# Kernel tuning notes

Hardware: AMD Instinct MI355X
Metric: run time of the kernel (lower is better)

## Reference

```python
import jax, jax.numpy as jnp
import numpy as np

SIGNAL = (32, 32)
KERNEL = (8, 8)
N_FEATURES = [64, 128, 128]
BATCH = 64
ALPHA = 0.5          # source references an undefined global `alpha`; fixed here
LEAKY_SLOPE = 0.01   # torch F.leaky_relu default


def _join_tensor(S, K, loc):
    i = np.arange(S)[:, None, None]
    j = np.arange(S)[None, :, None]
    k = np.arange(K)[None, None, :]
    M = (j >= i) & (i == np.maximum(j, k + loc))
    return jnp.asarray(M.astype(np.float32))


def _meet_tensor(S, K, loc):
    i = np.arange(S)[:, None, None]
    j = np.arange(S)[None, :, None]
    k = np.arange(K)[None, None, :]
    M = (j >= i) & (i == np.minimum(j, k + loc))
    return jnp.asarray(M.astype(np.float32))


def setup_inputs() -> dict:
    key = jax.random.key(0)
    sx, sy = SIGNAL
    kx, ky = KERNEL
    # meet layers use kernel_loc = signal - kernel; join layers use (0, 0)
    cmx = _meet_tensor(sx, kx, sx - kx)
    cmy = _meet_tensor(sy, ky, sy - ky)
    cjx = _join_tensor(sx, kx, 0)
    cjy = _join_tensor(sy, ky, 0)

    keys = jax.random.split(key, 16)
    x = jax.random.normal(keys[0], (BATCH, N_FEATURES[0], sx, sy), dtype=jnp.float32)

    def kaiming(k, shape):
        fan_in = shape[0] * shape[1] * shape[2]  # kx*ky*in_features
        return jax.random.normal(k, shape, dtype=jnp.float32) * np.float32(np.sqrt(2.0 / fan_in))

    inp = {"x": x, "cmx": cmx, "cmy": cmy, "cjx": cjx, "cjy": cjy}
    for li in range(len(N_FEATURES) - 1):
        fi, fo = N_FEATURES[li], N_FEATURES[li + 1]
        inp[f"mw{li}"] = kaiming(keys[1 + 2 * li], (kx, ky, fi, fo))
        inp[f"mb{li}"] = jnp.zeros((fo, 1, 1), dtype=jnp.float32)
        inp[f"jw{li}"] = kaiming(keys[2 + 2 * li], (kx, ky, fi, fo))
        inp[f"jb{li}"] = jnp.zeros((fo, 1, 1), dtype=jnp.float32)
    return inp


def _lattice_conv(cx, cy, X, W, b):
    # Y[m,g,x,y] = sum_{i,j,a,b} cx[i,x,a] cy[j,y,b] X[m,f,i,j] W[a,b,f,g] + bias
    return jnp.einsum('ixa,jyb,mfij,abfg->mgxy', cx, cy, X, W, optimize='optimal') + b


def reference(x, cmx, cmy, cjx, cjy, mw0, mb0, jw0, jb0, mw1, mb1, jw1, jb1):
    params = [(mw0, mb0, jw0, jb0), (mw1, mb1, jw1, jb1)]
    for mw, mb, jw, jb in params:
        m = _lattice_conv(cmx, cmy, x, mw, mb)
        j = _lattice_conv(cjx, cjy, x, jw, jb)
        x = jax.nn.leaky_relu((1.0 - ALPHA) * m + ALPHA * j, negative_slope=LEAKY_SLOPE)
    return x
```

## Files before the change

kernel.cpp:

```cpp
#include <hip/hip_runtime.h>
#include <stdint.h>


typedef __attribute__((ext_vector_type(8))) short short8;
typedef __attribute__((ext_vector_type(4))) float floatx4;

__device__ __forceinline__ float bf2f(unsigned short u) {
  union { uint32_t u; float f; } c; c.u = ((uint32_t)u) << 16; return c.f;
}
__device__ __forceinline__ unsigned short f2bf(float f) {
  union { float f; uint32_t u; } c; c.f = f;
  uint32_t u = c.u;
  uint32_t r = (u + 0x7FFFu + ((u >> 16) & 1u)) >> 16;
  return (unsigned short)r;
}

__device__ __forceinline__ int detect_fp32_block(
    const unsigned short* __restrict__ xa, int* scnt) {
  if (threadIdx.x == 0) *scnt = 0;
  __syncthreads();
  unsigned short v = xa[threadIdx.x & 255];
  int e = (v >> 7) & 0xFF;
  int ok = (v == 0) || (e >= 110 && e <= 140);
  atomicAdd(scnt, ok);
  __syncthreads();
  return (*scnt >= 240) ? 0 : 1;
}

#define SLOT_W1 0
#define SLOT_SB 225
#define SLOT_AS 289
#define SLOT_M  353
#define N_SLOTS 417
#define N_SLOTS_PAD 448

__global__ __launch_bounds__(256) void mega_setup(
    const unsigned short* __restrict__ xa,
    const void* __restrict__ mw0, const void* __restrict__ jw0,
    const void* __restrict__ mw1, const void* __restrict__ jw1,
    const void* __restrict__ mb0, const void* __restrict__ jb0,
    const void* __restrict__ mb1, const void* __restrict__ jb1,
    unsigned short* __restrict__ L, float* __restrict__ bias0,
    float* __restrict__ bias1, unsigned short* __restrict__ PBg0,
    unsigned short* __restrict__ PBg1, unsigned short* __restrict__ Xt0) {
  __shared__ unsigned short shbuf[128 * 33];
  __shared__ int scnt;
  int blk = blockIdx.x;

  if (blk < 224) {
    int tid = blk * 256 + threadIdx.x;
    int slot = tid >> 7, k = tid & 127;
    int isj = k >= 64, ab = k & 63, a = ab >> 3, b = ab & 7;
    float v = 0.f;
    if (slot < 225) {
      int cx = slot / 15, cy = slot % 15;
      int pmx = cx < 7 ? cx : 7, pxx = cx > 7 ? cx - 7 : 0;
      int pmy = cy < 7 ? cy : 7, pyy = cy > 7 ? cy - 7 : 0;
      if (!isj) v = (a >= pxx && b >= pyy) ? 0.5f : 0.f;
      else      v = (a <= pmx && b <= pmy) ? 0.5f : 0.f;
    } else if (slot < 289) {
      int s = slot - SLOT_SB, px = s >> 3, b0 = s & 7;
      if (!isj) v = (a >= px && b == b0) ? 0.5f : 0.f;
    } else if (slot < 353) {
      int s = slot - SLOT_AS, a0 = s >> 3, py = s & 7;
      if (!isj) v = (a == a0 && b >= py) ? 0.5f : 0.f;
    } else if (slot < 417) {
      int s = slot - SLOT_M, a0 = s >> 3, b0 = s & 7;
      if (!isj) v = (a == a0 && b == b0) ? 0.5f : 0.f;
    }
    L[tid] = f2bf(v);
    return;
  }

  if (blk == 224) {
    int fp32 = detect_fp32_block(xa, &scnt);
    int g = threadIdx.x & 127;
    const void* mb = (threadIdx.x < 128) ? mb0 : mb1;
    const void* jb = (threadIdx.x < 128) ? jb0 : jb1;
    float* bo = (threadIdx.x < 128) ? bias0 : bias1;
    float m = fp32 ? ((const float*)mb)[g] : bf2f(((const unsigned short*)mb)[g]);
    float j = fp32 ? ((const float*)jb)[g] : bf2f(((const unsigned short*)jb)[g]);
    bo[g] = 0.5f * (m + j);
    return;
  }

  int tx = threadIdx.x & 31, ty = threadIdx.x >> 5;

  if (blk < 1249) {
    int fp32 = detect_fp32_block(xa, &scnt);
    int pblk = blk - 225;
    int layer = pblk >> 9;
    int rem = pblk & 511;
    int f = rem >> 2, gt = rem & 3;
    int F = layer ? 128 : 64;
    if (f >= F) return;
    int g0 = gt * 32;
    const int G = 128, FG = F * G;
    const void* mw = layer ? mw1 : mw0;
    const void* jw = layer ? jw1 : jw0;
    unsigned short* PB = layer ? PBg1 : PBg0;
    for (int k = ty; k < 128; k += 8) {
      const void* src = (k < 64) ? mw : jw;
      int ab = k & 63;
      size_t idx = (size_t)ab * FG + (size_t)f * G + g0 + tx;
      shbuf[k * 33 + tx] = fp32 ? f2bf(((const float*)src)[idx])
                                : ((const unsigned short*)src)[idx];
    }
    __syncthreads();
    int kk = threadIdx.x & 127, gs = threadIdx.x >> 7;
    for (int gg = gs; gg < 32; gg += 2)
      PB[((size_t)(g0 + gg) * F + f) * 128 + kk] = shbuf[kk * 33 + gg];
    return;
  }

  {
    int fp32 = detect_fp32_block(xa, &scnt);
    int tblk = blk - 1249;
    int c0 = (tblk & 31) * 32, r0 = (tblk >> 5) * 32;
    const int R = 4096, C = 1024;
    if (fp32) {
#pragma unroll
      for (int i = 0; i < 32; i += 8)
        shbuf[(ty + i) * 33 + tx] =
            f2bf(((const float*)xa)[(size_t)(r0 + ty + i) * C + (c0 + tx)]);
    } else {
#pragma unroll
      for (int i = 0; i < 32; i += 8)
        shbuf[(ty + i) * 33 + tx] = xa[(size_t)(r0 + ty + i) * C + (c0 + tx)];
    }
    __syncthreads();
#pragma unroll
    for (int i = 0; i < 32; i += 8)
      Xt0[(size_t)(c0 + ty + i) * R + (r0 + tx)] = shbuf[tx * 33 + ty + i];
  }
}

template <int F, int NT>
__device__ __forceinline__ void mfma_tile(
    const unsigned short* __restrict__ A, const unsigned short* __restrict__ W,
    floatx4 acc[NT], int wave, int n, int q) {
  const unsigned short* a_ptr = A + ((size_t)(wave * 16 + n)) * F + q * 8;
  const unsigned short* w_ptr = W + (size_t)n * F + q * 8;
#pragma unroll
  for (int kk = 0; kk < F; kk += 32) {
    short8 av = *(const short8*)(a_ptr + kk);
#pragma unroll
    for (int t = 0; t < NT; ++t) {
      short8 bv = *(const short8*)(w_ptr + (size_t)t * 16 * F + kk);
      acc[t] = __builtin_amdgcn_mfma_f32_16x16x32_bf16(av, bv, acc[t], 0, 0, 0);
    }
  }
}

__global__ __launch_bounds__(256) void prep_gemm2(
    const unsigned short* __restrict__ L,
    const unsigned short* __restrict__ PBg0,
    const unsigned short* __restrict__ PBg1,
    unsigned short* __restrict__ Wall0, unsigned short* __restrict__ Wall1) {
  int layer = blockIdx.z;
  int GF = layer ? 16384 : 8192;
  int n0 = blockIdx.x * 128;
  if (n0 >= GF) return;
  int m0 = blockIdx.y * 64;
  const unsigned short* PB = layer ? PBg1 : PBg0;
  unsigned short* Wall = layer ? Wall1 : Wall0;
  int wave = threadIdx.x >> 6, lane = threadIdx.x & 63;
  int n = lane & 15, q = lane >> 4;
  floatx4 acc[8];
#pragma unroll
  for (int t = 0; t < 8; ++t) acc[t] = (floatx4){0.f, 0.f, 0.f, 0.f};
  mfma_tile<128, 8>(L + (size_t)m0 * 128, PB + (size_t)n0 * 128, acc, wave, n, q);
#pragma unroll
  for (int t = 0; t < 8; ++t) {
    int gcol = n0 + t * 16 + n;
#pragma unroll
    for (int r = 0; r < 4; ++r) {
      int m = m0 + wave * 16 + q * 4 + r;
      Wall[(size_t)m * GF + gcol] = f2bf(acc[t][r]);
    }
  }
}

template <int F>
__global__ __launch_bounds__(256) void corr_gemm(
    const unsigned short* __restrict__ Xt, const unsigned short* __restrict__ Wall,
    unsigned short* __restrict__ V, unsigned short* __restrict__ U,
    unsigned short* __restrict__ T) {
  int bid = blockIdx.x, gs = blockIdx.y;
  int wave = threadIdx.x >> 6, lane = threadIdx.x & 63;
  int n = lane & 15, q = lane >> 4;
  int ipos, slot;
  unsigned short* out;
  if (bid < 256) {
    int a = bid >> 5, y = bid & 31;
    int py = y > 24 ? y - 24 : 0;
    ipos = (24 + a) * 32 + y;
    slot = SLOT_AS + a * 8 + py;
    out = V + (size_t)(a * 32 + y) * 8192;
  } else if (bid < 512) {
    int i = bid - 256;
    int b = i >> 5, x = i & 31;
    int px = x > 24 ? x - 24 : 0;
    ipos = x * 32 + 24 + b;
    slot = SLOT_SB + px * 8 + b;
    out = U + (size_t)(b * 32 + x) * 8192;
  } else {
    int i = bid - 512;
    int a = i >> 3, b = i & 7;
    ipos = (24 + a) * 32 + 24 + b;
    slot = SLOT_M + a * 8 + b;
    out = T + (size_t)(a * 8 + b) * 8192;
  }
  floatx4 acc[4];
#pragma unroll
  for (int t = 0; t < 4; ++t) acc[t] = (floatx4){0.f, 0.f, 0.f, 0.f};
  mfma_tile<F, 4>(Xt + (size_t)ipos * 64 * F,
                  Wall + ((size_t)slot * 128 + gs * 64) * F, acc, wave, n, q);
#pragma unroll
  for (int t = 0; t < 4; ++t) {
    int gcol = gs * 64 + t * 16 + n;
#pragma unroll
    for (int r = 0; r < 4; ++r) {
      int m = wave * 16 + q * 4 + r;
      out[(size_t)m * 128 + gcol] = f2bf(acc[t][r]);
    }
  }
}

template <int F>
__global__ __launch_bounds__(256) void final_gemm(
    const unsigned short* __restrict__ Xt, const unsigned short* __restrict__ Wall,
    const unsigned short* __restrict__ V, const unsigned short* __restrict__ U,
    const unsigned short* __restrict__ T, const float* __restrict__ bias,
    unsigned short* __restrict__ Out) {
  int pos = blockIdx.x, gs = blockIdx.y;
  int x = pos >> 5, y = pos & 31;
  int wave = threadIdx.x >> 6, lane = threadIdx.x & 63;
  int n = lane & 15, q = lane >> 4;
  int clsx = x < 7 ? x : (x <= 24 ? 7 : x - 17);
  int clsy = y < 7 ? y : (y <= 24 ? 7 : y - 17);
  int px = x > 24 ? x - 24 : 0;
  int py = y > 24 ? y - 24 : 0;

  int rowoff[4], coloff[4];
#pragma unroll
  for (int r = 0; r < 4; ++r) rowoff[r] = (wave * 16 + q * 4 + r) * 128;
#pragma unroll
  for (int t = 0; t < 4; ++t) coloff[t] = gs * 64 + t * 16 + n;

  float csum[4][4];
#pragma unroll
  for (int t = 0; t < 4; ++t) {
    float bv = bias[coloff[t]];
#pragma unroll
    for (int r = 0; r < 4; ++r) csum[t][r] = bv;
  }
  for (int a = 0; a < px; ++a) {
    const unsigned short* p = V + (size_t)(a * 32 + y) * 8192;
#pragma unroll
    for (int t = 0; t < 4; ++t)
#pragma unroll
      for (int r = 0; r < 4; ++r) csum[t][r] += bf2f(p[rowoff[r] + coloff[t]]);
  }
  for (int b = 0; b < py; ++b) {
    const unsigned short* p = U + (size_t)(b * 32 + x) * 8192;
#pragma unroll
    for (int t = 0; t < 4; ++t)
#pragma unroll
      for (int r = 0; r < 4; ++r) csum[t][r] += bf2f(p[rowoff[r] + coloff[t]]);
  }
  for (int a = 0; a < px; ++a)
    for (int b = 0; b < py; ++b) {
      const unsigned short* p = T + (size_t)(a * 8 + b) * 8192;
#pragma unroll
      for (int t = 0; t < 4; ++t)
#pragma unroll
        for (int r = 0; r < 4; ++r) csum[t][r] += bf2f(p[rowoff[r] + coloff[t]]);
    }

  floatx4 acc[4];
#pragma unroll
  for (int t = 0; t < 4; ++t) acc[t] = (floatx4){0.f, 0.f, 0.f, 0.f};
  mfma_tile<F, 4>(Xt + (size_t)pos * 64 * F,
                  Wall + ((size_t)(SLOT_W1 + clsx * 15 + clsy) * 128 + gs * 64) * F,
                  acc, wave, n, q);

  unsigned short* o = Out + (size_t)pos * 64 * 128;
#pragma unroll
  for (int t = 0; t < 4; ++t) {
#pragma unroll
    for (int r = 0; r < 4; ++r) {
      float v = acc[t][r] + csum[t][r];
      v = v > 0.f ? v : 0.01f * v;
      o[rowoff[r] + coloff[t]] = f2bf(v);
    }
  }
}

__global__ __launch_bounds__(256) void transpose_out(
    const unsigned short* __restrict__ xa, const unsigned short* __restrict__ src,
    unsigned short* __restrict__ d16, float* __restrict__ d32) {
  __shared__ unsigned short tile[32][33];
  __shared__ int scnt;
  int fp32 = detect_fp32_block(xa, &scnt);
  const int R = 1024, C = 8192;
  int tx = threadIdx.x & 31, ty = threadIdx.x >> 5;
  int c0 = blockIdx.x * 32, r0 = blockIdx.y * 32;
#pragma unroll
  for (int i = 0; i < 32; i += 8)
    tile[ty + i][tx] = src[(size_t)(r0 + ty + i) * C + (c0 + tx)];
  __syncthreads();
  if (fp32) {
#pragma unroll
    for (int i = 0; i < 32; i += 8)
      d32[(size_t)(c0 + ty + i) * R + (r0 + tx)] = bf2f(tile[tx][ty + i]);
  } else {
#pragma unroll
    for (int i = 0; i < 32; i += 8)
      d16[(size_t)(c0 + ty + i) * R + (r0 + tx)] = tile[tx][ty + i];
  }
}

extern "C" void kernel_launch(void* const* d_in, const int* in_sizes, int n_in,
                              void* d_out, int out_size, void* d_ws,
                              size_t ws_size, hipStream_t stream) {
  const void* x   = d_in[0];
  const void* mw0 = d_in[5];
  const void* mb0 = d_in[6];
  const void* jw0 = d_in[7];
  const void* jb0 = d_in[8];
  const void* mw1 = d_in[9];
  const void* mb1 = d_in[10];
  const void* jw1 = d_in[11];
  const void* jb1 = d_in[12];

  char* ws = (char*)d_ws;
  const size_t MB = 1u << 20;
  unsigned short* Xt0   = (unsigned short*)(ws + 0);
  unsigned short* A1    = (unsigned short*)(ws + 9 * MB);
  unsigned short* Wall0 = (unsigned short*)(ws + 26 * MB);
  unsigned short* Wall1 = (unsigned short*)(ws + 34 * MB);
  unsigned short* Out2  = (unsigned short*)(ws + 49 * MB);
  unsigned short* PBg0  = (unsigned short*)(ws + 66 * MB);
  unsigned short* PBg1  = (unsigned short*)(ws + 69 * MB);
  unsigned short* L     = (unsigned short*)(ws + 74 * MB);
  float* bias0 = (float*)(ws + 75 * MB);
  float* bias1 = bias0 + 128;
  unsigned short* V = (unsigned short*)(ws + 76 * MB);
  unsigned short* U = (unsigned short*)(ws + 81 * MB);
  unsigned short* T = (unsigned short*)(ws + 86 * MB);

  mega_setup<<<5345, 256, 0, stream>>>(
      (const unsigned short*)x, mw0, jw0, mw1, jw1, mb0, jb0, mb1, jb1, L,
      bias0, bias1, PBg0, PBg1, Xt0);
  prep_gemm2<<<dim3(128, 7, 2), 256, 0, stream>>>(L, PBg0, PBg1, Wall0, Wall1);

  corr_gemm<64><<<dim3(576, 2), 256, 0, stream>>>(Xt0, Wall0, V, U, T);
  final_gemm<64><<<dim3(1024, 2), 256, 0, stream>>>(Xt0, Wall0, V, U, T,
                                                    bias0, A1);
  corr_gemm<128><<<dim3(576, 2), 256, 0, stream>>>(A1, Wall1, V, U, T);
  final_gemm<128><<<dim3(1024, 2), 256, 0, stream>>>(A1, Wall1, V, U, T,
                                                     bias1, Out2);

  transpose_out<<<dim3(256, 32), 256, 0, stream>>>(
      (const unsigned short*)x, Out2, (unsigned short*)d_out, (float*)d_out);
}
```

Before: 270.0 us.

## Prefix-sum correction tensors so final GEMM reads one entry each

```diff
diff --git a/kernel.cpp b/kernel.cpp
--- a/kernel.cpp
+++ b/kernel.cpp
@@ -227,6 +227,39 @@
   }
 }
 
+__global__ __launch_bounds__(256) void scan_corr(unsigned short* __restrict__ V,
+                                                 unsigned short* __restrict__ U,
+                                                 unsigned short* __restrict__ T) {
+  int b = blockIdx.x;
+  if (b < 2048) {
+    unsigned short* base = (b < 1024) ? V : U;
+    int tid = ((b & 1023) * 256 + threadIdx.x);
+    unsigned short* p = base + (size_t)tid;
+    float s = 0.f;
+#pragma unroll
+    for (int a = 0; a < 8; ++a) {
+      s += bf2f(p[(size_t)a * 262144]);
+      p[(size_t)a * 262144] = f2bf(s);
+    }
+  } else {
+    int mg = (b - 2048) * 256 + threadIdx.x;
+    float col[8];
+#pragma unroll
+    for (int i = 0; i < 8; ++i) col[i] = 0.f;
+#pragma unroll
+    for (int a = 0; a < 8; ++a) {
+      float rs = 0.f;
+#pragma unroll
+      for (int bb = 0; bb < 8; ++bb) {
+        size_t idx = (size_t)(a * 8 + bb) * 8192 + mg;
+        col[bb] += bf2f(T[idx]);
+        rs += col[bb];
+        T[idx] = f2bf(rs);
+      }
+    }
+  }
+}
+
 template <int F>
 __global__ __launch_bounds__(256) void final_gemm(
     const unsigned short* __restrict__ Xt, const unsigned short* __restrict__ Wall,
@@ -241,42 +274,27 @@
   int clsy = y < 7 ? y : (y <= 24 ? 7 : y - 17);
   int px = x > 24 ? x - 24 : 0;
   int py = y > 24 ? y - 24 : 0;
-
-  int rowoff[4], coloff[4];
-#pragma unroll
-  for (int r = 0; r < 4; ++r) rowoff[r] = (wave * 16 + q * 4 + r) * 128;
-#pragma unroll
-  for (int t = 0; t < 4; ++t) coloff[t] = gs * 64 + t * 16 + n;
+  const unsigned short* c3 = px ? V + ((size_t)(px - 1) * 32 + y) * 8192 : nullptr;
+  const unsigned short* c2 = py ? U + ((size_t)(py - 1) * 32 + x) * 8192 : nullptr;
+  const unsigned short* c4 =
+      (px && py) ? T + (size_t)((px - 1) * 8 + (py - 1)) * 8192 : nullptr;
 
   float csum[4][4];
 #pragma unroll
   for (int t = 0; t < 4; ++t) {
-    float bv = bias[coloff[t]];
-#pragma unroll
-    for (int r = 0; r < 4; ++r) csum[t][r] = bv;
-  }
-  for (int a = 0; a < px; ++a) {
-    const unsigned short* p = V + (size_t)(a * 32 + y) * 8192;
-#pragma unroll
-    for (int t = 0; t < 4; ++t)
-#pragma unroll
-      for (int r = 0; r < 4; ++r) csum[t][r] += bf2f(p[rowoff[r] + coloff[t]]);
-  }
-  for (int b = 0; b < py; ++b) {
-    const unsigned short* p = U + (size_t)(b * 32 + x) * 8192;
-#pragma unroll
-    for (int t = 0; t < 4; ++t)
-#pragma unroll
-      for (int r = 0; r < 4; ++r) csum[t][r] += bf2f(p[rowoff[r] + coloff[t]]);
-  }
-  for (int a = 0; a < px; ++a)
-    for (int b = 0; b < py; ++b) {
-      const unsigned short* p = T + (size_t)(a * 8 + b) * 8192;
-#pragma unroll
-      for (int t = 0; t < 4; ++t)
-#pragma unroll
-        for (int r = 0; r < 4; ++r) csum[t][r] += bf2f(p[rowoff[r] + coloff[t]]);
-    }
+    int gcol = gs * 64 + t * 16 + n;
+    float bv = bias[gcol];
+#pragma unroll
+    for (int r = 0; r < 4; ++r) {
+      int m = wave * 16 + q * 4 + r;
+      size_t idx = (size_t)m * 128 + gcol;
+      float v = bv;
+      if (c3) v += bf2f(c3[idx]);
+      if (c2) v += bf2f(c2[idx]);
+      if (c4) v += bf2f(c4[idx]);
+      csum[t][r] = v;
+    }
+  }
 
   floatx4 acc[4];
 #pragma unroll
@@ -288,11 +306,13 @@
   unsigned short* o = Out + (size_t)pos * 64 * 128;
 #pragma unroll
   for (int t = 0; t < 4; ++t) {
+    int gcol = gs * 64 + t * 16 + n;
 #pragma unroll
     for (int r = 0; r < 4; ++r) {
+      int m = wave * 16 + q * 4 + r;
       float v = acc[t][r] + csum[t][r];
       v = v > 0.f ? v : 0.01f * v;
-      o[rowoff[r] + coloff[t]] = f2bf(v);
+      o[(size_t)m * 128 + gcol] = f2bf(v);
     }
   }
 }
@@ -356,9 +376,11 @@
   prep_gemm2<<<dim3(128, 7, 2), 256, 0, stream>>>(L, PBg0, PBg1, Wall0, Wall1);
 
   corr_gemm<64><<<dim3(576, 2), 256, 0, stream>>>(Xt0, Wall0, V, U, T);
+  scan_corr<<<2080, 256, 0, stream>>>(V, U, T);
   final_gemm<64><<<dim3(1024, 2), 256, 0, stream>>>(Xt0, Wall0, V, U, T,
                                                     bias0, A1);
   corr_gemm<128><<<dim3(576, 2), 256, 0, stream>>>(A1, Wall1, V, U, T);
+  scan_corr<<<2080, 256, 0, stream>>>(V, U, T);
   final_gemm<128><<<dim3(1024, 2), 256, 0, stream>>>(A1, Wall1, V, U, T,
                                                      bias1, Out2);
 
```

Result: faster. 257.8 us (-4.5%).
